# Kernel tuning notes

Measured on AMD Instinct MI355X. Metric: run time of the kernel, lower is better.

Reference implementation:

```python
import jax, jax.numpy as jnp
import numpy as np


def setup_inputs() -> dict:
    key = jax.random.key(0)
    kx, ky = jax.random.split(key)
    x = jax.random.normal(kx, (8, 4096, 3), dtype=jnp.float32)
    y = jax.random.normal(ky, (8, 4096, 3), dtype=jnp.float32)
    return {"x": x, "y": y}


def reference(x, y):
    # Mathematically identical to sum((x[:, :, None] - y[:, None, :])**2, -1)
    # but avoids materializing the [B, n, m, 3] diff tensor.
    x2 = jnp.sum(x * x, axis=-1)              # [B, n]
    y2 = jnp.sum(y * y, axis=-1)              # [B, m]
    xy = jnp.einsum('bnd,bmd->bnm', x, y)     # [B, n, m]
    dist = x2[:, :, None] + y2[:, None, :] - 2.0 * xy  # [B, n, m]
    min_dist_xy = jnp.min(dist, axis=2)       # [B, n] nearest y for each x
    min_dist_yx = jnp.min(dist, axis=1)       # [B, m] nearest x for each y
    return jnp.mean(min_dist_xy, axis=1) + jnp.mean(min_dist_yx, axis=1)  # [B]
```

## Files before the change

### kernel.cpp

```cpp
#include <hip/hip_runtime.h>
#include <math.h>

#define BLK 256
#define NX 8
#define XT 2
#define NPTS 4096
#define YLEN 256
#define CCH (NPTS / YLEN)
#define UNITS 65536

__global__ __launch_bounds__(BLK, 2) void chamfer_partial_kernel(
    const float* __restrict__ X, const float* __restrict__ Y,
    float* __restrict__ partial, float* __restrict__ out)
{
  __shared__ float4 sh[YLEN];

  int lin = blockIdx.x;
  int c   = lin % CCH; lin /= CCH;
  int xt  = lin % XT;  lin /= XT;
  int b   = lin & 7;
  int dir = lin >> 3;

  const float* xs = (dir ? Y : X) + b * (NPTS * 3);
  const float* ys = (dir ? X : Y) + b * (NPTS * 3);

  if (blockIdx.x == 0 && threadIdx.x < 8) out[threadIdx.x] = 0.0f;

  {
    int j = threadIdx.x;
    float y0 = ys[(c * YLEN + j) * 3 + 0];
    float y1 = ys[(c * YLEN + j) * 3 + 1];
    float y2 = ys[(c * YLEN + j) * 3 + 2];
    sh[j] = make_float4(y0, y1, y2, 0.5f * (y0 * y0 + y1 * y1 + y2 * y2));
  }
  __syncthreads();

  int x0i = xt * (BLK * NX) + threadIdx.x * NX;
  float xf[NX * 3];
  {
    const float4* xp = reinterpret_cast<const float4*>(xs + x0i * 3);
    #pragma unroll
    for (int i = 0; i < 6; ++i) {
      float4 p = xp[i];
      xf[i * 4 + 0] = p.x; xf[i * 4 + 1] = p.y;
      xf[i * 4 + 2] = p.z; xf[i * 4 + 3] = p.w;
    }
  }
  float n0[NX], n1[NX], n2[NX], x2h[NX], gm[NX];
  #pragma unroll
  for (int k = 0; k < NX; ++k) {
    float a = xf[k * 3 + 0], bb = xf[k * 3 + 1], cc = xf[k * 3 + 2];
    n0[k] = -a; n1[k] = -bb; n2[k] = -cc;
    x2h[k] = 0.5f * (a * a + bb * bb + cc * cc);
    gm[k] = __builtin_inff();
  }

  #pragma unroll 4
  for (int j = 0; j < YLEN; j += 4) {
    float4 p0 = sh[j], p1 = sh[j + 1], p2 = sh[j + 2], p3 = sh[j + 3];
    #pragma unroll
    for (int k = 0; k < NX; ++k) {
      float ga = fmaf(n0[k], p0.x, fmaf(n1[k], p0.y, fmaf(n2[k], p0.z, p0.w)));
      float gb = fmaf(n0[k], p1.x, fmaf(n1[k], p1.y, fmaf(n2[k], p1.z, p1.w)));
      float gc = fmaf(n0[k], p2.x, fmaf(n1[k], p2.y, fmaf(n2[k], p2.z, p2.w)));
      float gd = fmaf(n0[k], p3.x, fmaf(n1[k], p3.y, fmaf(n2[k], p3.z, p3.w)));
      float m  = fminf(fminf(ga, gb), gc);
      gm[k] = fminf(fminf(m, gd), gm[k]);
    }
  }

  float* dst = partial + (size_t)c * UNITS + dir * 32768 + b * 4096 + x0i;
  float4* d4 = reinterpret_cast<float4*>(dst);
  d4[0] = make_float4(2.0f * (x2h[0] + gm[0]), 2.0f * (x2h[1] + gm[1]),
                      2.0f * (x2h[2] + gm[2]), 2.0f * (x2h[3] + gm[3]));
  d4[1] = make_float4(2.0f * (x2h[4] + gm[4]), 2.0f * (x2h[5] + gm[5]),
                      2.0f * (x2h[6] + gm[6]), 2.0f * (x2h[7] + gm[7]));
}

__global__ __launch_bounds__(BLK, 4) void chamfer_reduce_kernel(
    const float* __restrict__ partial, float* __restrict__ out)
{
  int b = blockIdx.x >> 5;
  int s = blockIdx.x & 31;
  int i = s * BLK + threadIdx.x;
  int dir = i >> 12;
  int xi  = i & 4095;
  int unit = dir * 32768 + b * 4096 + xi;
  float v0 = __builtin_inff(), v1 = v0, v2 = v0, v3 = v0;
  float v4 = v0, v5 = v0, v6 = v0, v7 = v0;
  #pragma unroll
  for (int c = 0; c < CCH; c += 8) {
    v0 = fminf(v0, partial[(size_t)(c + 0) * UNITS + unit]);
    v1 = fminf(v1, partial[(size_t)(c + 1) * UNITS + unit]);
    v2 = fminf(v2, partial[(size_t)(c + 2) * UNITS + unit]);
    v3 = fminf(v3, partial[(size_t)(c + 3) * UNITS + unit]);
    v4 = fminf(v4, partial[(size_t)(c + 4) * UNITS + unit]);
    v5 = fminf(v5, partial[(size_t)(c + 5) * UNITS + unit]);
    v6 = fminf(v6, partial[(size_t)(c + 6) * UNITS + unit]);
    v7 = fminf(v7, partial[(size_t)(c + 7) * UNITS + unit]);
  }
  float v = fminf(fminf(fminf(v0, v1), fminf(v2, v3)),
                  fminf(fminf(v4, v5), fminf(v6, v7)));
  #pragma unroll
  for (int off = 32; off > 0; off >>= 1) v += __shfl_down(v, off, 64);
  __shared__ float wsum[BLK / 64];
  if ((threadIdx.x & 63) == 0) wsum[threadIdx.x >> 6] = v;
  __syncthreads();
  if (threadIdx.x == 0) {
    float t = wsum[0] + wsum[1] + wsum[2] + wsum[3];
    atomicAdd(&out[b], t * (1.0f / 4096.0f));
  }
}

__global__ __launch_bounds__(BLK, 2) void chamfer_direct_kernel(
    const float* __restrict__ X, const float* __restrict__ Y,
    float* __restrict__ out)
{
  extern __shared__ float4 shd[];
  int lin = blockIdx.x;
  int xt  = lin & 1;  lin >>= 1;
  int b   = lin & 7;
  int dir = lin >> 3;
  const float* xs = (dir ? Y : X) + b * (NPTS * 3);
  const float* ys = (dir ? X : Y) + b * (NPTS * 3);

  for (int j = threadIdx.x; j < NPTS; j += BLK) {
    float y0 = ys[j * 3 + 0], y1 = ys[j * 3 + 1], y2 = ys[j * 3 + 2];
    shd[j] = make_float4(y0, y1, y2, 0.5f * (y0 * y0 + y1 * y1 + y2 * y2));
  }
  __syncthreads();

  int x0i = xt * (BLK * 8) + threadIdx.x * 8;
  float xf[24];
  const float4* xp = reinterpret_cast<const float4*>(xs + x0i * 3);
  #pragma unroll
  for (int i = 0; i < 6; ++i) {
    float4 p = xp[i];
    xf[i * 4 + 0] = p.x; xf[i * 4 + 1] = p.y;
    xf[i * 4 + 2] = p.z; xf[i * 4 + 3] = p.w;
  }
  float n0[8], n1[8], n2[8], x2h[8], gm[8];
  #pragma unroll
  for (int k = 0; k < 8; ++k) {
    float a = xf[k * 3 + 0], bb = xf[k * 3 + 1], cc = xf[k * 3 + 2];
    n0[k] = -a; n1[k] = -bb; n2[k] = -cc;
    x2h[k] = 0.5f * (a * a + bb * bb + cc * cc);
    gm[k] = __builtin_inff();
  }
  for (int j = 0; j < NPTS; j += 4) {
    float4 p0 = shd[j], p1 = shd[j + 1], p2 = shd[j + 2], p3 = shd[j + 3];
    #pragma unroll
    for (int k = 0; k < 8; ++k) {
      float ga = fmaf(n0[k], p0.x, fmaf(n1[k], p0.y, fmaf(n2[k], p0.z, p0.w)));
      float gb = fmaf(n0[k], p1.x, fmaf(n1[k], p1.y, fmaf(n2[k], p1.z, p1.w)));
      float gc = fmaf(n0[k], p2.x, fmaf(n1[k], p2.y, fmaf(n2[k], p2.z, p2.w)));
      float gd = fmaf(n0[k], p3.x, fmaf(n1[k], p3.y, fmaf(n2[k], p3.z, p3.w)));
      float m  = fminf(fminf(ga, gb), gc);
      gm[k] = fminf(fminf(m, gd), gm[k]);
    }
  }
  float v = 0.0f;
  #pragma unroll
  for (int k = 0; k < 8; ++k) v += 2.0f * (x2h[k] + gm[k]);
  #pragma unroll
  for (int off = 32; off > 0; off >>= 1) v += __shfl_down(v, off, 64);
  __syncthreads();
  float* red = reinterpret_cast<float*>(shd);
  if ((threadIdx.x & 63) == 0) red[threadIdx.x >> 6] = v;
  __syncthreads();
  if (threadIdx.x == 0) {
    float s = red[0] + red[1] + red[2] + red[3];
    atomicAdd(&out[b], s * (1.0f / 4096.0f));
  }
}

__global__ void zero_out_kernel(float* out)
{
  if (threadIdx.x < 8) out[threadIdx.x] = 0.0f;
}

extern "C" void kernel_launch(void* const* d_in, const int* in_sizes, int n_in,
                              void* d_out, int out_size, void* d_ws, size_t ws_size,
                              hipStream_t stream)
{
  const float* X = (const float*)d_in[0];
  const float* Y = (const float*)d_in[1];
  float* out = (float*)d_out;

  if (ws_size >= (size_t)CCH * UNITS * sizeof(float)) {
    chamfer_partial_kernel<<<2 * 8 * XT * CCH, BLK, 0, stream>>>(
        X, Y, (float*)d_ws, out);
    chamfer_reduce_kernel<<<256, BLK, 0, stream>>>((const float*)d_ws, out);
  } else {
    zero_out_kernel<<<1, 64, 0, stream>>>(out);
    chamfer_direct_kernel<<<2 * 8 * 2, BLK, NPTS * sizeof(float4), stream>>>(
        X, Y, out);
  }
}
```

Baseline: 80.74 us.

## Fuse partial min and reduce via in-block y-slicing with shuffle min

Each block now loads all 4096 y points into a 64KB shared buffer with an XOR swizzle. Within the block, 16 lanes each scan a 256-point slice for the same 8 x points, and the lanes combine their minima through shuffle-xor. This removes the 4MB partial-min workspace write and read, the separate reduce pass, and the atomics, replacing them with per-block sums and a tiny deterministic final kernel. The costs are more shared-memory traffic per block and lower occupancy from the 64KB LDS allocation, and each block repeats the full y load.

Result: no change. 79.96 us (-1.0%).

```diff
diff --git a/kernel.cpp b/kernel.cpp
--- a/kernel.cpp
+++ b/kernel.cpp
@@ -3,39 +3,37 @@
 
 #define BLK 256
 #define NX 8
-#define XT 2
 #define NPTS 4096
-#define YLEN 256
-#define CCH (NPTS / YLEN)
-#define UNITS 65536
-
-__global__ __launch_bounds__(BLK, 2) void chamfer_partial_kernel(
+#define SLICES 16
+#define SLICE 256
+#define XT 32
+#define XPB 128
+
+__global__ __launch_bounds__(BLK, 2) void chamfer_fused_kernel(
     const float* __restrict__ X, const float* __restrict__ Y,
-    float* __restrict__ partial, float* __restrict__ out)
-{
-  __shared__ float4 sh[YLEN];
+    float* __restrict__ sums)
+{
+  __shared__ float4 sh[NPTS];
 
   int lin = blockIdx.x;
-  int c   = lin % CCH; lin /= CCH;
-  int xt  = lin % XT;  lin /= XT;
+  int xt  = lin & 31; lin >>= 5;
   int b   = lin & 7;
   int dir = lin >> 3;
 
   const float* xs = (dir ? Y : X) + b * (NPTS * 3);
   const float* ys = (dir ? X : Y) + b * (NPTS * 3);
 
-  if (blockIdx.x == 0 && threadIdx.x < 8) out[threadIdx.x] = 0.0f;
-
-  {
-    int j = threadIdx.x;
-    float y0 = ys[(c * YLEN + j) * 3 + 0];
-    float y1 = ys[(c * YLEN + j) * 3 + 1];
-    float y2 = ys[(c * YLEN + j) * 3 + 2];
-    sh[j] = make_float4(y0, y1, y2, 0.5f * (y0 * y0 + y1 * y1 + y2 * y2));
-  }
-  __syncthreads();
-
-  int x0i = xt * (BLK * NX) + threadIdx.x * NX;
+  int t = threadIdx.x;
+
+  #pragma unroll
+  for (int r = 0; r < SLICES; ++r) {
+    const float* yp = ys + (r * SLICE + t) * 3;
+    float y0 = yp[0], y1 = yp[1], y2 = yp[2];
+    sh[r * SLICE + (t ^ (r & 7))] =
+        make_float4(y0, y1, y2, 0.5f * (y0 * y0 + y1 * y1 + y2 * y2));
+  }
+
+  int x0i = xt * XPB + (t >> 4) * NX;
   float xf[NX * 3];
   {
     const float4* xp = reinterpret_cast<const float4*>(xs + x0i * 3);
@@ -55,61 +53,67 @@
     gm[k] = __builtin_inff();
   }
 
-  #pragma unroll 4
-  for (int j = 0; j < YLEN; j += 4) {
-    float4 p0 = sh[j], p1 = sh[j + 1], p2 = sh[j + 2], p3 = sh[j + 3];
+  __syncthreads();
+
+  int s  = t & 15;
+  int mk = s & 7;
+  const float4* sp = sh + s * SLICE;
+  int o0 = 0 ^ mk, o1 = 1 ^ mk, o2 = 2 ^ mk, o3 = 3 ^ mk;
+  int o4 = 4 ^ mk, o5 = 5 ^ mk, o6 = 6 ^ mk, o7 = 7 ^ mk;
+
+  #pragma unroll 2
+  for (int w = 0; w < SLICE; w += 8) {
+    float4 p0 = sp[w + o0], p1 = sp[w + o1], p2 = sp[w + o2], p3 = sp[w + o3];
+    float4 p4 = sp[w + o4], p5 = sp[w + o5], p6 = sp[w + o6], p7 = sp[w + o7];
     #pragma unroll
     for (int k = 0; k < NX; ++k) {
-      float ga = fmaf(n0[k], p0.x, fmaf(n1[k], p0.y, fmaf(n2[k], p0.z, p0.w)));
-      float gb = fmaf(n0[k], p1.x, fmaf(n1[k], p1.y, fmaf(n2[k], p1.z, p1.w)));
-      float gc = fmaf(n0[k], p2.x, fmaf(n1[k], p2.y, fmaf(n2[k], p2.z, p2.w)));
-      float gd = fmaf(n0[k], p3.x, fmaf(n1[k], p3.y, fmaf(n2[k], p3.z, p3.w)));
-      float m  = fminf(fminf(ga, gb), gc);
-      gm[k] = fminf(fminf(m, gd), gm[k]);
+      float g0 = fmaf(n0[k], p0.x, fmaf(n1[k], p0.y, fmaf(n2[k], p0.z, p0.w)));
+      float g1 = fmaf(n0[k], p1.x, fmaf(n1[k], p1.y, fmaf(n2[k], p1.z, p1.w)));
+      float g2 = fmaf(n0[k], p2.x, fmaf(n1[k], p2.y, fmaf(n2[k], p2.z, p2.w)));
+      float g3 = fmaf(n0[k], p3.x, fmaf(n1[k], p3.y, fmaf(n2[k], p3.z, p3.w)));
+      float g4 = fmaf(n0[k], p4.x, fmaf(n1[k], p4.y, fmaf(n2[k], p4.z, p4.w)));
+      float g5 = fmaf(n0[k], p5.x, fmaf(n1[k], p5.y, fmaf(n2[k], p5.z, p5.w)));
+      float g6 = fmaf(n0[k], p6.x, fmaf(n1[k], p6.y, fmaf(n2[k], p6.z, p6.w)));
+      float g7 = fmaf(n0[k], p7.x, fmaf(n1[k], p7.y, fmaf(n2[k], p7.z, p7.w)));
+      float m0 = fminf(fminf(g0, g1), g2);
+      float m1 = fminf(fminf(g3, g4), g5);
+      float m2 = fminf(fminf(m0, m1), g6);
+      gm[k]    = fminf(fminf(m2, g7), gm[k]);
     }
   }
 
-  float* dst = partial + (size_t)c * UNITS + dir * 32768 + b * 4096 + x0i;
-  float4* d4 = reinterpret_cast<float4*>(dst);
-  d4[0] = make_float4(2.0f * (x2h[0] + gm[0]), 2.0f * (x2h[1] + gm[1]),
-                      2.0f * (x2h[2] + gm[2]), 2.0f * (x2h[3] + gm[3]));
-  d4[1] = make_float4(2.0f * (x2h[4] + gm[4]), 2.0f * (x2h[5] + gm[5]),
-                      2.0f * (x2h[6] + gm[6]), 2.0f * (x2h[7] + gm[7]));
-}
-
-__global__ __launch_bounds__(BLK, 4) void chamfer_reduce_kernel(
-    const float* __restrict__ partial, float* __restrict__ out)
-{
-  int b = blockIdx.x >> 5;
-  int s = blockIdx.x & 31;
-  int i = s * BLK + threadIdx.x;
-  int dir = i >> 12;
-  int xi  = i & 4095;
-  int unit = dir * 32768 + b * 4096 + xi;
-  float v0 = __builtin_inff(), v1 = v0, v2 = v0, v3 = v0;
-  float v4 = v0, v5 = v0, v6 = v0, v7 = v0;
-  #pragma unroll
-  for (int c = 0; c < CCH; c += 8) {
-    v0 = fminf(v0, partial[(size_t)(c + 0) * UNITS + unit]);
-    v1 = fminf(v1, partial[(size_t)(c + 1) * UNITS + unit]);
-    v2 = fminf(v2, partial[(size_t)(c + 2) * UNITS + unit]);
-    v3 = fminf(v3, partial[(size_t)(c + 3) * UNITS + unit]);
-    v4 = fminf(v4, partial[(size_t)(c + 4) * UNITS + unit]);
-    v5 = fminf(v5, partial[(size_t)(c + 5) * UNITS + unit]);
-    v6 = fminf(v6, partial[(size_t)(c + 6) * UNITS + unit]);
-    v7 = fminf(v7, partial[(size_t)(c + 7) * UNITS + unit]);
-  }
-  float v = fminf(fminf(fminf(v0, v1), fminf(v2, v3)),
-                  fminf(fminf(v4, v5), fminf(v6, v7)));
-  #pragma unroll
-  for (int off = 32; off > 0; off >>= 1) v += __shfl_down(v, off, 64);
-  __shared__ float wsum[BLK / 64];
-  if ((threadIdx.x & 63) == 0) wsum[threadIdx.x >> 6] = v;
-  __syncthreads();
-  if (threadIdx.x == 0) {
-    float t = wsum[0] + wsum[1] + wsum[2] + wsum[3];
-    atomicAdd(&out[b], t * (1.0f / 4096.0f));
-  }
+  #pragma unroll
+  for (int mm = 1; mm < 16; mm <<= 1) {
+    #pragma unroll
+    for (int k = 0; k < NX; ++k)
+      gm[k] = fminf(gm[k], __shfl_xor(gm[k], mm, 64));
+  }
+
+  float v = 0.0f;
+  #pragma unroll
+  for (int k = 0; k < NX; ++k) v += 2.0f * (x2h[k] + gm[k]);
+  if (s != 0) v = 0.0f;
+  #pragma unroll
+  for (int mm = 1; mm < 64; mm <<= 1) v += __shfl_xor(v, mm, 64);
+
+  __syncthreads();
+  float* red = reinterpret_cast<float*>(sh);
+  if ((t & 63) == 0) red[t >> 6] = v;
+  __syncthreads();
+  if (t == 0) sums[blockIdx.x] = red[0] + red[1] + red[2] + red[3];
+}
+
+__global__ __launch_bounds__(512) void chamfer_final_kernel(
+    const float* __restrict__ sums, float* __restrict__ out)
+{
+  __shared__ float gred[16];
+  int t = threadIdx.x;
+  float v = sums[t];
+  #pragma unroll
+  for (int mm = 1; mm < 32; mm <<= 1) v += __shfl_xor(v, mm, 64);
+  if ((t & 31) == 0) gred[t >> 5] = v;
+  __syncthreads();
+  if (t < 8) out[t] = (gred[t] + gred[t + 8]) * (1.0f / 4096.0f);
 }
 
 __global__ __launch_bounds__(BLK, 2) void chamfer_direct_kernel(
@@ -169,8 +173,8 @@
   if ((threadIdx.x & 63) == 0) red[threadIdx.x >> 6] = v;
   __syncthreads();
   if (threadIdx.x == 0) {
-    float s = red[0] + red[1] + red[2] + red[3];
-    atomicAdd(&out[b], s * (1.0f / 4096.0f));
+    float s2 = red[0] + red[1] + red[2] + red[3];
+    atomicAdd(&out[b], s2 * (1.0f / 4096.0f));
   }
 }
 
@@ -187,10 +191,9 @@
   const float* Y = (const float*)d_in[1];
   float* out = (float*)d_out;
 
-  if (ws_size >= (size_t)CCH * UNITS * sizeof(float)) {
-    chamfer_partial_kernel<<<2 * 8 * XT * CCH, BLK, 0, stream>>>(
-        X, Y, (float*)d_ws, out);
-    chamfer_reduce_kernel<<<256, BLK, 0, stream>>>((const float*)d_ws, out);
+  if (ws_size >= (size_t)(2 * 8 * XT) * sizeof(float)) {
+    chamfer_fused_kernel<<<2 * 8 * XT, BLK, 0, stream>>>(X, Y, (float*)d_ws);
+    chamfer_final_kernel<<<1, 512, 0, stream>>>((const float*)d_ws, out);
   } else {
     zero_out_kernel<<<1, 64, 0, stream>>>(out);
     chamfer_direct_kernel<<<2 * 8 * 2, BLK, NPTS * sizeof(float4), stream>>>(
```
